# Kernel tuning notes

Hardware: AMD Instinct MI355X
Metric: run time of the kernel (lower is better)

The kernel has to match this reference:

```python
import jax, jax.numpy as jnp
import numpy as np

B, S, D = 8, 4096, 1280   # batch, tokens, model width (== down_dim == out_dim)
R = 64                    # lora rank (mid_dim)
EMBED_W = D + R * R + D   # [down | mid | up] slices of the per-sample embed


def setup_inputs() -> dict:
    key = jax.random.key(0)
    ks = jax.random.split(key, 6)
    x = jax.random.normal(ks[0], (B, S, D), dtype=jnp.float32)
    embed = jax.random.normal(ks[1], (B, EMBED_W), dtype=jnp.float32) * 0.05
    w_down = jax.random.normal(ks[2], (R, D), dtype=jnp.float32) * 0.02
    b_down = jnp.zeros((R,), dtype=jnp.float32)
    w_up = jax.random.normal(ks[3], (D, R), dtype=jnp.float32) * 0.02
    b_up = jnp.zeros((D,), dtype=jnp.float32)
    return {"x": x, "embed": embed, "w_down": w_down, "b_down": b_down,
            "w_up": w_up, "b_up": b_up}


def reference(x, embed, w_down, b_down, w_up, b_up):
    # down_forward: modulate input channels by per-sample down weight, then lora_down
    down_w = embed[:, :D]                          # [B, D]
    h = x * down_w[:, None, :]                     # [B, S, D]
    h = jnp.einsum('bsd,rd->bsr', h, w_down) + b_down   # lora_down Linear(D->R)
    # mid_forward: per-sample [R,R] weight, x_chunk @ W.T  (batched, no python loop)
    mid_w = embed[:, D:D + R * R].reshape(B, R, R)       # [B, R, R]
    h = jnp.einsum('bsr,bqr->bsq', h, mid_w)             # [B, S, R]
    # up_forward: lora_up then modulate output channels by per-sample up weight
    out = jnp.einsum('bsr,dr->bsd', h, w_up) + b_up      # lora_up Linear(R->D)
    up_w = embed[:, -D:]                                 # [B, D]
    out = out * up_w[:, None, :]
    return out
```

## Files before the change

kernel.cpp:

```cpp
#include <hip/hip_runtime.h>
#include <hip/hip_bf16.h>

#define NB 8
#define NS 4096
#define ND 1280
#define NR 64
#define EW 6656

#define AS1 __attribute__((address_space(1)))
#define AS3 __attribute__((address_space(3)))

typedef __attribute__((ext_vector_type(4))) float f4;
typedef __attribute__((ext_vector_type(8))) short bf8;

union BF8U { bf8 v; unsigned u[4]; };

__device__ __forceinline__ unsigned short f2bf(float f) {
  union { float f; unsigned u; } v; v.f = f;
  unsigned u = v.u + 0x7FFFu + ((v.u >> 16) & 1u);
  return (unsigned short)(u >> 16);
}

__device__ __forceinline__ unsigned pk2(float a, float b) {
  __hip_bfloat162 t = __float22bfloat162_rn(float2{a, b});
  return *reinterpret_cast<unsigned*>(&t);
}

__global__ __launch_bounds__(256) void prep_all(const float* __restrict__ embed,
                                                const float* __restrict__ w_down,
                                                const float* __restrict__ w_up,
                                                const float* __restrict__ b_down,
                                                unsigned short* __restrict__ W2F,
                                                unsigned short* __restrict__ W3FB,
                                                float* __restrict__ h2bias) {
  const int blk = blockIdx.x;
  const int t   = threadIdx.x;
  if (blk < 160) {
    const int b  = blk / 20;
    const int qg = (blk % 20) / 5;
    const int dg = blk % 5;
    __shared__ float mids[16][64];
    #pragma unroll
    for (int i = 0; i < 4; ++i) {
      int idx = t + i * 256;
      mids[idx >> 6][idx & 63] = embed[b * EW + ND + qg * 1024 + idx];
    }
    __syncthreads();
    const int d = dg * 256 + t;
    float acc[16];
    #pragma unroll
    for (int q = 0; q < 16; ++q) acc[q] = 0.f;
    for (int r = 0; r < 64; r += 8) {
      float wd[8];
      #pragma unroll
      for (int u = 0; u < 8; ++u) wd[u] = w_down[(r + u) * ND + d];
      #pragma unroll
      for (int u = 0; u < 8; ++u)
        #pragma unroll
        for (int q = 0; q < 16; ++q) acc[q] += mids[q][r + u] * wd[u];
    }
    const float dwn = embed[b * EW + d];
    const int kt = d >> 5, lanehi = (d & 31) >> 3, jj = d & 7;
    #pragma unroll
    for (int q = 0; q < 16; ++q)
      W2F[(((b * 40 + kt) * 4 + qg) << 9) + (lanehi * 16 + q) * 8 + jj] = f2bf(acc[q] * dwn);
  } else if (blk < 2720) {
    const int local = blk - 160;
    const int b  = local / 320;
    const int g  = (local % 320) * 256 + t;
    const int d  = g >> 6, q = g & 63;
    const int kt = q >> 5, dt = d >> 4;
    const int lanei = ((q & 31) >> 3) * 16 + (d & 15), jj = q & 7;
    const float upw = embed[b * EW + 5376 + d];
    W3FB[(size_t)b * 81920 + ((kt * 80 + dt) * 64 + lanei) * 8 + jj] = f2bf(w_up[g] * upw);
  } else {
    #pragma unroll
    for (int ii = 0; ii < 2; ++ii) {
      int id = ii * 256 + t;
      int bb = id >> 6, q = id & 63;
      float s = 0.f;
      for (int r = 0; r < 64; ++r) s += b_down[r] * embed[bb * EW + ND + q * 64 + r];
      h2bias[id] = s;
    }
  }
}

__global__ __launch_bounds__(512, 4) void kA(const float* __restrict__ x,
                                             const unsigned short* __restrict__ W2F,
                                             const float* __restrict__ h2bias,
                                             unsigned* __restrict__ h2F) {
  const int tid  = threadIdx.x;
  const int lane = tid & 63;
  const int w    = tid >> 6;
  const int b    = blockIdx.x >> 8;
  const int tile = blockIdx.x & 255;
  const int lo16 = lane & 15;
  const int hi4  = lane >> 4;

  __shared__ __align__(16) char pool[33856];
  float (*xs)[16][260]  = (float (*)[16][260])pool;
  float (*part)[16][66] = (float (*)[16][66])pool;

  const float* xrow0 = x + ((size_t)b * NS + tile * 16) * ND;
  const unsigned short* w2b = W2F + (size_t)b * 81920;

  #define DMA_A(c, buf)                                                              \
    _Pragma("unroll")                                                                \
    for (int i = 0; i < 2; ++i) {                                                    \
      const int r = 2 * w + i;                                                       \
      const float* src = xrow0 + (size_t)r * ND + (c) * 256 + lane * 4;              \
      __builtin_amdgcn_global_load_lds((AS1 void*)src,                               \
          (AS3 void*)&xs[buf][r][0], 16, 0, 0);                                      \
    }

  DMA_A(0, 0)

  f4 acc[4] = {};
  for (int c = 0; c < 5; ++c) {
    const int buf = c & 1;
    asm volatile("s_waitcnt vmcnt(0)" ::: "memory");
    __syncthreads();
    const int kt = c * 8 + w;
    const unsigned short* wp = w2b + ((kt * 4) << 9) + lane * 8;
    bf8 bw0 = *(const bf8*)(wp);
    bf8 bw1 = *(const bf8*)(wp + (1 << 9));
    bf8 bw2 = *(const bf8*)(wp + (2 << 9));
    bf8 bw3 = *(const bf8*)(wp + (3 << 9));
    if (c < 4) DMA_A(c + 1, buf ^ 1)
    f4 a0 = *(const f4*)&xs[buf][lo16][w * 32 + hi4 * 8];
    f4 a1 = *(const f4*)&xs[buf][lo16][w * 32 + hi4 * 8 + 4];
    BF8U af;
    af.u[0] = pk2(a0[0], a0[1]); af.u[1] = pk2(a0[2], a0[3]);
    af.u[2] = pk2(a1[0], a1[1]); af.u[3] = pk2(a1[2], a1[3]);
    acc[0] = __builtin_amdgcn_mfma_f32_16x16x32_bf16(af.v, bw0, acc[0], 0, 0, 0);
    acc[1] = __builtin_amdgcn_mfma_f32_16x16x32_bf16(af.v, bw1, acc[1], 0, 0, 0);
    acc[2] = __builtin_amdgcn_mfma_f32_16x16x32_bf16(af.v, bw2, acc[2], 0, 0, 0);
    acc[3] = __builtin_amdgcn_mfma_f32_16x16x32_bf16(af.v, bw3, acc[3], 0, 0, 0);
  }

  __syncthreads();

  #pragma unroll
  for (int nt = 0; nt < 4; ++nt)
    #pragma unroll
    for (int j = 0; j < 4; ++j)
      part[w][hi4 * 4 + j][nt * 16 + lo16] = acc[nt][j];
  __syncthreads();

  {
    const int s  = tid >> 5;
    const int q0 = (tid & 31) * 2;
    float v0 = h2bias[b * 64 + q0];
    float v1 = h2bias[b * 64 + q0 + 1];
    #pragma unroll
    for (int ww = 0; ww < 8; ++ww) {
      v0 += part[ww][s][q0];
      v1 += part[ww][s][q0 + 1];
    }
    const unsigned pk = pk2(v0, v1);
    const int kt2   = q0 >> 5;
    const int lanei = ((q0 & 31) >> 3) * 16 + s;
    const int u     = (q0 & 7) >> 1;
    h2F[(size_t)blockIdx.x * 512 + (kt2 * 64 + lanei) * 4 + u] = pk;
  }
}

__global__ __launch_bounds__(512, 2) void kB(const unsigned* __restrict__ h2F,
                                             const float* __restrict__ embed,
                                             const float* __restrict__ b_up,
                                             const unsigned short* __restrict__ W3FB,
                                             float* __restrict__ out) {
  const int tid  = threadIdx.x;
  const int lane = tid & 63;
  const int w    = tid >> 6;
  const int b    = blockIdx.x >> 8;
  const int tile = blockIdx.x & 255;
  const int lo16 = lane & 15;
  const int hi4  = lane >> 4;

  __shared__ __align__(16) float outS[16][1284];
  __shared__ __align__(16) float pbs[1280];

  {
    const float* upw = embed + b * EW + 5376;
    for (int i = tid; i < 1280; i += 512) pbs[i] = b_up[i] * upw[i];
  }

  BF8U ha0, ha1;
  {
    const unsigned* hp = h2F + (size_t)blockIdx.x * 512;
    uint4 h0 = *(const uint4*)(hp + (0 * 64 + lane) * 4);
    uint4 h1 = *(const uint4*)(hp + (1 * 64 + lane) * 4);
    ha0.u[0] = h0.x; ha0.u[1] = h0.y; ha0.u[2] = h0.z; ha0.u[3] = h0.w;
    ha1.u[0] = h1.x; ha1.u[1] = h1.y; ha1.u[2] = h1.z; ha1.u[3] = h1.w;
  }

  const unsigned short* w3b = W3FB + (size_t)b * 81920;

  int dt = w * 10;
  bf8 wb0 = *(const bf8*)(w3b + (size_t)(dt * 64 + lane) * 8);
  bf8 wb1 = *(const bf8*)(w3b + (size_t)((80 + dt) * 64 + lane) * 8);

  for (int i = 0; i < 10; ++i) {
    bf8 wn0, wn1;
    if (i < 9) {
      wn0 = *(const bf8*)(w3b + (size_t)((dt + 1) * 64 + lane) * 8);
      wn1 = *(const bf8*)(w3b + (size_t)((80 + dt + 1) * 64 + lane) * 8);
    }
    f4 o = {};
    o = __builtin_amdgcn_mfma_f32_16x16x32_bf16(wb0, ha0.v, o, 0, 0, 0);
    o = __builtin_amdgcn_mfma_f32_16x16x32_bf16(wb1, ha1.v, o, 0, 0, 0);
    *(f4*)&outS[lo16][dt * 16 + hi4 * 4] = o;
    wb0 = wn0; wb1 = wn1;
    ++dt;
  }

  __syncthreads();

  #pragma unroll
  for (int i = 0; i < 2; ++i) {
    const int r = 2 * w + i;
    float* orow = out + ((size_t)b * NS + tile * 16 + r) * ND;
    #pragma unroll
    for (int c = 0; c < 5; ++c) {
      const int col = c * 256 + lane * 4;
      f4 v = *(const f4*)&outS[r][col];
      f4 p = *(const f4*)&pbs[col];
      f4 rr;
      #pragma unroll
      for (int j = 0; j < 4; ++j) rr[j] = v[j] + p[j];
      *(f4*)(orow + col) = rr;
    }
  }
}

extern "C" void kernel_launch(void* const* d_in, const int* in_sizes, int n_in,
                              void* d_out, int out_size, void* d_ws, size_t ws_size,
                              hipStream_t stream) {
  const float* x      = (const float*)d_in[0];
  const float* embed  = (const float*)d_in[1];
  const float* w_down = (const float*)d_in[2];
  const float* b_down = (const float*)d_in[3];
  const float* w_up   = (const float*)d_in[4];
  const float* b_up   = (const float*)d_in[5];
  float* out = (float*)d_out;

  char* ws = (char*)d_ws;
  unsigned short* W2F  = (unsigned short*)ws;
  unsigned short* W3FB = (unsigned short*)(ws + 1310720);
  float* h2bias        = (float*)(ws + 2621440);
  unsigned* h2F        = (unsigned*)(ws + 2623488);

  prep_all<<<2721, 256, 0, stream>>>(embed, w_down, w_up, b_down, W2F, W3FB, h2bias);
  kA<<<2048, 512, 0, stream>>>(x, W2F, h2bias, h2F);
  kB<<<2048, 512, 0, stream>>>(h2F, embed, b_up, W3FB, out);
}
```

Before: 113.6 us.

## Deepen kA x-tile prefetch to four LDS buffers with partial vmcnt waits

Replaces the double-buffered loop in kernel kA with a fully unrolled schedule that keeps up to three x chunks in flight across four LDS buffers. The bf16 weight fragments are prefetched one step ahead into registers, and fine-grained s_waitcnt vmcnt counts replace full drains. The aim is to hide global-load latency behind the MFMA work. In exchange, LDS use roughly doubles, the row pitch changes from 260 to 268 floats, and more registers are held, which may lower occupancy under launch_bounds(512,4). Correctness depends on the hand-counted vmcnt values and on raw s_barrier without a compiler fence.

```diff
diff --git a/kernel.cpp b/kernel.cpp
--- a/kernel.cpp
+++ b/kernel.cpp
@@ -97,8 +97,8 @@
   const int lo16 = lane & 15;
   const int hi4  = lane >> 4;
 
-  __shared__ __align__(16) char pool[33856];
-  float (*xs)[16][260]  = (float (*)[16][260])pool;
+  __shared__ __align__(16) char pool[68608];
+  float (*xs)[16][268]  = (float (*)[16][268])pool;
   float (*part)[16][66] = (float (*)[16][66])pool;
 
   const float* xrow0 = x + ((size_t)b * NS + tile * 16) * ND;
@@ -113,30 +113,59 @@
           (AS3 void*)&xs[buf][r][0], 16, 0, 0);                                      \
     }
 
+  #define LOADB(dst, c) {                                                            \
+    const unsigned short* wp = w2b + ((((c) * 8 + w) * 4) << 9) + lane * 8;          \
+    dst[0] = *(const bf8*)(wp);                                                      \
+    dst[1] = *(const bf8*)(wp + (1 << 9));                                           \
+    dst[2] = *(const bf8*)(wp + (2 << 9));                                           \
+    dst[3] = *(const bf8*)(wp + (3 << 9));                                           \
+  }
+
+  #define COMPUTE(c, bwX) {                                                          \
+    f4 a0 = *(const f4*)&xs[(c) & 3][lo16][w * 32 + hi4 * 8];                        \
+    f4 a1 = *(const f4*)&xs[(c) & 3][lo16][w * 32 + hi4 * 8 + 4];                    \
+    BF8U af;                                                                         \
+    af.u[0] = pk2(a0[0], a0[1]); af.u[1] = pk2(a0[2], a0[3]);                        \
+    af.u[2] = pk2(a1[0], a1[1]); af.u[3] = pk2(a1[2], a1[3]);                        \
+    acc[0] = __builtin_amdgcn_mfma_f32_16x16x32_bf16(af.v, bwX[0], acc[0], 0, 0, 0); \
+    acc[1] = __builtin_amdgcn_mfma_f32_16x16x32_bf16(af.v, bwX[1], acc[1], 0, 0, 0); \
+    acc[2] = __builtin_amdgcn_mfma_f32_16x16x32_bf16(af.v, bwX[2], acc[2], 0, 0, 0); \
+    acc[3] = __builtin_amdgcn_mfma_f32_16x16x32_bf16(af.v, bwX[3], acc[3], 0, 0, 0); \
+  }
+
+  f4 acc[4] = {};
+  bf8 b0f[4], b1f[4], b2f[4], b3f[4], b4f[4];
+
   DMA_A(0, 0)
-
-  f4 acc[4] = {};
-  for (int c = 0; c < 5; ++c) {
-    const int buf = c & 1;
-    asm volatile("s_waitcnt vmcnt(0)" ::: "memory");
-    __syncthreads();
-    const int kt = c * 8 + w;
-    const unsigned short* wp = w2b + ((kt * 4) << 9) + lane * 8;
-    bf8 bw0 = *(const bf8*)(wp);
-    bf8 bw1 = *(const bf8*)(wp + (1 << 9));
-    bf8 bw2 = *(const bf8*)(wp + (2 << 9));
-    bf8 bw3 = *(const bf8*)(wp + (3 << 9));
-    if (c < 4) DMA_A(c + 1, buf ^ 1)
-    f4 a0 = *(const f4*)&xs[buf][lo16][w * 32 + hi4 * 8];
-    f4 a1 = *(const f4*)&xs[buf][lo16][w * 32 + hi4 * 8 + 4];
-    BF8U af;
-    af.u[0] = pk2(a0[0], a0[1]); af.u[1] = pk2(a0[2], a0[3]);
-    af.u[2] = pk2(a1[0], a1[1]); af.u[3] = pk2(a1[2], a1[3]);
-    acc[0] = __builtin_amdgcn_mfma_f32_16x16x32_bf16(af.v, bw0, acc[0], 0, 0, 0);
-    acc[1] = __builtin_amdgcn_mfma_f32_16x16x32_bf16(af.v, bw1, acc[1], 0, 0, 0);
-    acc[2] = __builtin_amdgcn_mfma_f32_16x16x32_bf16(af.v, bw2, acc[2], 0, 0, 0);
-    acc[3] = __builtin_amdgcn_mfma_f32_16x16x32_bf16(af.v, bw3, acc[3], 0, 0, 0);
-  }
+  DMA_A(1, 1)
+  LOADB(b0f, 0)
+  DMA_A(2, 2)
+  LOADB(b1f, 1)
+
+  asm volatile("s_waitcnt vmcnt(6)" ::: "memory");
+  __builtin_amdgcn_s_barrier();
+  DMA_A(3, 3)
+  LOADB(b2f, 2)
+  COMPUTE(0, b0f)
+
+  asm volatile("s_waitcnt vmcnt(6)" ::: "memory");
+  __builtin_amdgcn_s_barrier();
+  DMA_A(4, 0)
+  LOADB(b3f, 3)
+  COMPUTE(1, b1f)
+
+  asm volatile("s_waitcnt vmcnt(6)" ::: "memory");
+  __builtin_amdgcn_s_barrier();
+  LOADB(b4f, 4)
+  COMPUTE(2, b2f)
+
+  asm volatile("s_waitcnt vmcnt(4)" ::: "memory");
+  __builtin_amdgcn_s_barrier();
+  COMPUTE(3, b3f)
+
+  asm volatile("s_waitcnt vmcnt(0)" ::: "memory");
+  __builtin_amdgcn_s_barrier();
+  COMPUTE(4, b4f)
 
   __syncthreads();
 
```

New measurement: 112.7 us. About the same (-0.8%).

## Load full x row tile into LDS at once and prefetch B fragments in registers

Applied to the files above, without the earlier changes.

kA now issues all five K-chunks of the 16x1280 x tile as LDS DMA up front into a single 82 KB buffer, removing the per-chunk double-buffer waits and block barriers. The W2 fragments for the next chunk are register-prefetched while the current chunk's MFMAs run. This cuts synchronization and exposes more memory-level parallelism. The cost is much larger LDS per block, with launch bounds lowered to 2 blocks per SM, so occupancy drops.

```diff
diff --git a/kernel.cpp b/kernel.cpp
--- a/kernel.cpp
+++ b/kernel.cpp
@@ -85,7 +85,7 @@
   }
 }
 
-__global__ __launch_bounds__(512, 4) void kA(const float* __restrict__ x,
+__global__ __launch_bounds__(512, 2) void kA(const float* __restrict__ x,
                                              const unsigned short* __restrict__ W2F,
                                              const float* __restrict__ h2bias,
                                              unsigned* __restrict__ h2F) {
@@ -97,45 +97,53 @@
   const int lo16 = lane & 15;
   const int hi4  = lane >> 4;
 
-  __shared__ __align__(16) char pool[33856];
-  float (*xs)[16][260]  = (float (*)[16][260])pool;
+  __shared__ __align__(16) char pool[82176];
+  float (*xs)[1284]     = (float (*)[1284])pool;
   float (*part)[16][66] = (float (*)[16][66])pool;
 
   const float* xrow0 = x + ((size_t)b * NS + tile * 16) * ND;
   const unsigned short* w2b = W2F + (size_t)b * 81920;
 
-  #define DMA_A(c, buf)                                                              \
-    _Pragma("unroll")                                                                \
-    for (int i = 0; i < 2; ++i) {                                                    \
-      const int r = 2 * w + i;                                                       \
-      const float* src = xrow0 + (size_t)r * ND + (c) * 256 + lane * 4;              \
-      __builtin_amdgcn_global_load_lds((AS1 void*)src,                               \
-          (AS3 void*)&xs[buf][r][0], 16, 0, 0);                                      \
-    }
-
-  DMA_A(0, 0)
+  #define LOADB(dst, c) {                                                            \
+    const unsigned short* wp = w2b + ((((c) * 8 + w) * 4) << 9) + lane * 8;          \
+    dst[0] = *(const bf8*)(wp);                                                      \
+    dst[1] = *(const bf8*)(wp + (1 << 9));                                           \
+    dst[2] = *(const bf8*)(wp + (2 << 9));                                           \
+    dst[3] = *(const bf8*)(wp + (3 << 9));                                           \
+  }
+
+  #pragma unroll
+  for (int i = 0; i < 2; ++i) {
+    const int r = 2 * w + i;
+    #pragma unroll
+    for (int cc = 0; cc < 5; ++cc) {
+      const float* src = xrow0 + (size_t)r * ND + cc * 256 + lane * 4;
+      __builtin_amdgcn_global_load_lds((AS1 void*)src,
+                                       (AS3 void*)&xs[r][cc * 256], 16, 0, 0);
+    }
+  }
+
+  bf8 bw[4], bn[4];
+  LOADB(bw, 0)
+
+  asm volatile("s_waitcnt vmcnt(0)" ::: "memory");
+  __builtin_amdgcn_s_barrier();
 
   f4 acc[4] = {};
+  #pragma unroll
   for (int c = 0; c < 5; ++c) {
-    const int buf = c & 1;
-    asm volatile("s_waitcnt vmcnt(0)" ::: "memory");
-    __syncthreads();
-    const int kt = c * 8 + w;
-    const unsigned short* wp = w2b + ((kt * 4) << 9) + lane * 8;
-    bf8 bw0 = *(const bf8*)(wp);
-    bf8 bw1 = *(const bf8*)(wp + (1 << 9));
-    bf8 bw2 = *(const bf8*)(wp + (2 << 9));
-    bf8 bw3 = *(const bf8*)(wp + (3 << 9));
-    if (c < 4) DMA_A(c + 1, buf ^ 1)
-    f4 a0 = *(const f4*)&xs[buf][lo16][w * 32 + hi4 * 8];
-    f4 a1 = *(const f4*)&xs[buf][lo16][w * 32 + hi4 * 8 + 4];
+    if (c < 4) LOADB(bn, c + 1)
+    f4 a0 = *(const f4*)&xs[lo16][c * 256 + w * 32 + hi4 * 8];
+    f4 a1 = *(const f4*)&xs[lo16][c * 256 + w * 32 + hi4 * 8 + 4];
     BF8U af;
     af.u[0] = pk2(a0[0], a0[1]); af.u[1] = pk2(a0[2], a0[3]);
     af.u[2] = pk2(a1[0], a1[1]); af.u[3] = pk2(a1[2], a1[3]);
-    acc[0] = __builtin_amdgcn_mfma_f32_16x16x32_bf16(af.v, bw0, acc[0], 0, 0, 0);
-    acc[1] = __builtin_amdgcn_mfma_f32_16x16x32_bf16(af.v, bw1, acc[1], 0, 0, 0);
-    acc[2] = __builtin_amdgcn_mfma_f32_16x16x32_bf16(af.v, bw2, acc[2], 0, 0, 0);
-    acc[3] = __builtin_amdgcn_mfma_f32_16x16x32_bf16(af.v, bw3, acc[3], 0, 0, 0);
+    acc[0] = __builtin_amdgcn_mfma_f32_16x16x32_bf16(af.v, bw[0], acc[0], 0, 0, 0);
+    acc[1] = __builtin_amdgcn_mfma_f32_16x16x32_bf16(af.v, bw[1], acc[1], 0, 0, 0);
+    acc[2] = __builtin_amdgcn_mfma_f32_16x16x32_bf16(af.v, bw[2], acc[2], 0, 0, 0);
+    acc[3] = __builtin_amdgcn_mfma_f32_16x16x32_bf16(af.v, bw[3], acc[3], 0, 0, 0);
+    #pragma unroll
+    for (int i = 0; i < 4; ++i) bw[i] = bn[i];
   }
 
   __syncthreads();
```

Measured after the change: 123.2 us. 1.08x slower.
